# Optimization experiments

Measured on AMD Instinct MI355X. Metric: run time of the kernel, lower is better.

The kernel has to match this reference:

```python
import jax, jax.numpy as jnp
import numpy as np

B, N, C = 8, 16384, 80
MAX_OUT = 50
NEG = -1e30  # finite 'minus infinity' sentinel (safe under autodiff)


def setup_inputs() -> dict:
    key = jax.random.key(0)
    k1, k2 = jax.random.split(key)
    # two random corner points per box -> valid xyxy boxes in [0, 1000]
    pts = jax.random.uniform(k1, (B, N, 2, 2), dtype=jnp.float32) * 1000.0
    lo = jnp.min(pts, axis=2)
    hi = jnp.max(pts, axis=2)
    boxes = jnp.concatenate([lo, hi], axis=-1)  # [B, N, 4] (x1, y1, x2, y2)
    scores = jax.random.uniform(k2, (B, C, N), dtype=jnp.float32)
    return {
        "boxes": boxes,
        "scores": scores,
        "max_output_boxes_per_class": 50,
        "iou_threshold": jnp.array([0.5], dtype=jnp.float32),
        "score_threshold": jnp.array([0.5], dtype=jnp.float32),
    }


def _area(b):
    return (b[..., 2] - b[..., 0]) * (b[..., 3] - b[..., 1])


def _iou_one_vs_all(box, boxes):
    # box: [4], boxes: [N, 4] -> [N]
    x1 = jnp.maximum(box[0], boxes[:, 0])
    y1 = jnp.maximum(box[1], boxes[:, 1])
    x2 = jnp.minimum(box[2], boxes[:, 2])
    y2 = jnp.minimum(box[3], boxes[:, 3])
    inter = jnp.clip(x2 - x1, 0.0) * jnp.clip(y2 - y1, 0.0)
    union = _area(box) + _area(boxes) - inter
    return inter / jnp.maximum(union, 1e-9)


def _nms_single(boxes, scores, iou_thr, score_thr, max_out):
    # Greedy NMS for one (batch, class) lane. Returns [max_out] original box
    # indices in score-descending order, padded with -1.
    n = scores.shape[0]
    s0 = jnp.where(scores > score_thr, scores, NEG)  # score-threshold filter
    arange_n = jnp.arange(n)

    def step(s, _):
        idx = jnp.argmax(s)
        valid = s[idx] > (0.5 * NEG)  # any live candidate left?
        box = boxes[idx]
        iou = _iou_one_vs_all(box, boxes)
        sup = (iou > iou_thr) | (arange_n == idx)  # suppress overlaps + self
        s_new = jnp.where(valid & sup, NEG, s)
        return s_new, jnp.where(valid, idx, -1)

    _, idxs = jax.lax.scan(step, s0, None, length=max_out)
    return idxs  # [max_out] int32, -1 padded


def reference(boxes, scores, max_output_boxes_per_class, iou_threshold, score_threshold):
    b, c = scores.shape[0], scores.shape[1]
    iou_thr = iou_threshold[0]
    score_thr = score_threshold[0]
    max_out = int(max_output_boxes_per_class)

    per_class = lambda bx, sc: _nms_single(bx, sc, iou_thr, score_thr, max_out)
    nms_bc = jax.vmap(jax.vmap(per_class, in_axes=(None, 0)), in_axes=(0, 0))
    idxs = nms_bc(boxes, scores)  # [B, C, max_out]

    valid = idxs >= 0
    b_ids = jnp.broadcast_to(jnp.arange(b)[:, None, None], idxs.shape)
    c_ids = jnp.broadcast_to(jnp.arange(c)[None, :, None], idxs.shape)
    triples = jnp.stack(
        [jnp.where(valid, b_ids, -1), jnp.where(valid, c_ids, -1), idxs], axis=-1
    )
    # Padded equivalent of the dynamic [num_selected, 3] ONNX output:
    # rows with -1 are padding; valid rows are (batch, class, box) in the same
    # batch-major / class-major / score-descending order as the torch loop.
    return triples.reshape(-1, 3).astype(jnp.int64)
```

## Files before the change

### kernel.cpp

```cpp
#include <hip/hip_runtime.h>
#include <stdint.h>


#define NMS_B 8
#define NMS_N 16384
#define NMS_C 80
#define NMS_MAX_OUT 50
#define NTHREADS 256
#define NLANES (NMS_B * NMS_C)

#define OPT_THR 0.98828125f
#define FCAP 256
#define WMAX (FCAP / 64)
#define SPLIT 4
#define SEG 120
#define SCAN_N (NMS_N / SPLIT)

#define NBUCK 256
#define SCAP 1024
#define T_MIN 320

typedef unsigned long long u64;

#define WS_FLAGS  0
#define WS_CNTS   (NLANES * 4)
#define WS_TOTALS (WS_CNTS + NLANES * SPLIT * 4)
#define WS_KEYS   (WS_TOTALS + NLANES * SPLIT * 4)
#define WS_NEED   ((size_t)WS_KEYS + (size_t)NLANES * SPLIT * SEG * 8)

__device__ __forceinline__ float iou_exact(float4 A, float areaA, float4 Bx) {
    float x1 = fmaxf(A.x, Bx.x);
    float y1 = fmaxf(A.y, Bx.y);
    float x2 = fminf(A.z, Bx.z);
    float y2 = fminf(A.w, Bx.w);
    float dx = fmaxf(__fsub_rn(x2, x1), 0.0f);
    float dy = fmaxf(__fsub_rn(y2, y1), 0.0f);
    if (!(dx > 0.0f && dy > 0.0f)) return 0.0f;
    float inter = __fmul_rn(dx, dy);
    float areaB = __fmul_rn(__fsub_rn(Bx.z, Bx.x), __fsub_rn(Bx.w, Bx.y));
    float uni   = __fsub_rn(__fadd_rn(areaA, areaB), inter);
    return __fdiv_rn(inter, fmaxf(uni, 1e-9f));
}

__device__ __forceinline__ u64 umax64(u64 a, u64 b) { return a > b ? a : b; }
__device__ __forceinline__ u64 umin64(u64 a, u64 b) { return a < b ? a : b; }

__global__ __launch_bounds__(NTHREADS) void nms_scan(
    const float* __restrict__ scores,
    const float* __restrict__ p_sthr,
    int* __restrict__ cnts,
    int* __restrict__ totals,
    u64* __restrict__ keys)
{
    __shared__ u64 lkey[SEG];
    __shared__ int lcnt, ltot;

    const int bid  = blockIdx.x;
    const int bc   = bid / SPLIT;
    const int part = bid % SPLIT;
    const int tid  = threadIdx.x;

    const float4* sc4 = (const float4*)(scores + (size_t)bc * NMS_N + part * SCAN_N);
    float4 av[4];
    #pragma unroll
    for (int u = 0; u < 4; ++u) av[u] = sc4[u * NTHREADS + tid];
    __builtin_amdgcn_sched_barrier(0);

    if (tid == 0) { lcnt = 0; ltot = 0; }
    __syncthreads();

    const float sthr = p_sthr[0];
    int lt = 0;
    #pragma unroll
    for (int u = 0; u < 4; ++u) {
        const int i = u * NTHREADS + tid;
        float ss[4] = {av[u].x, av[u].y, av[u].z, av[u].w};
        #pragma unroll
        for (int j = 0; j < 4; ++j) {
            float s = ss[j];
            bool cand = (s > sthr);
            lt += cand ? 1 : 0;
            if (cand && s >= OPT_THR) {
                int n = part * SCAN_N + i * 4 + j;
                int p = atomicAdd(&lcnt, 1);
                if (p < SEG)
                    lkey[p] = ((u64)__float_as_uint(s) << 32)
                            | ((u64)(NMS_N - 1 - n) << 18);
            }
        }
    }
    #pragma unroll
    for (int off = 32; off > 0; off >>= 1) lt += __shfl_down(lt, off, 64);
    if ((tid & 63) == 0) atomicAdd(&ltot, lt);
    __syncthreads();

    const int cnt = lcnt;
    if (tid == 0) {
        cnts[bc * SPLIT + part]   = cnt;
        totals[bc * SPLIT + part] = ltot;
    }
    u64* kseg = keys + ((size_t)bc * SPLIT + part) * SEG;
    const int mm = (cnt < SEG) ? cnt : SEG;
    if (tid < mm) kseg[tid] = lkey[tid];
}

template <bool OUT64>
__global__ __launch_bounds__(64) void nms_sortwalk(
    const float* __restrict__ boxes,
    const int* __restrict__ p_maxout,
    const float* __restrict__ p_iou,
    void* __restrict__ out_raw,
    int* __restrict__ flags,
    const int* __restrict__ cnts,
    const int* __restrict__ totals,
    const u64* __restrict__ keys)
{
    __shared__ int    sn_[FCAP];
    __shared__ float4 sbox[FCAP];

    const int lane = threadIdx.x;
    const int bc   = blockIdx.x;
    const int b    = bc / NMS_C;
    const int c    = bc % NMS_C;

    const float iou_thr = p_iou[0];
    int maxo = p_maxout[0];
    if (maxo > NMS_MAX_OUT) maxo = NMS_MAX_OUT;
    if (maxo < 0) maxo = 0;

    int*       out32 = (int*)out_raw       + (size_t)bc * NMS_MAX_OUT * 3;
    long long* out64 = (long long*)out_raw + (size_t)bc * NMS_MAX_OUT * 3;
    #pragma unroll
    for (int i = lane; i < NMS_MAX_OUT * 3; i += 64) {
        if (OUT64) out64[i] = -1LL; else out32[i] = -1;
    }

    const int c0 = cnts[bc * SPLIT + 0], c1 = cnts[bc * SPLIT + 1];
    const int c2 = cnts[bc * SPLIT + 2], c3 = cnts[bc * SPLIT + 3];
    const int tt = totals[bc * SPLIT + 0] + totals[bc * SPLIT + 1]
                 + totals[bc * SPLIT + 2] + totals[bc * SPLIT + 3];
    const int o1 = c0, o2 = c0 + c1, o3 = c0 + c1 + c2;
    const int m  = o3 + c3;
    const bool bad = (c0 > SEG) | (c1 > SEG) | (c2 > SEG) | (c3 > SEG) | (m > FCAP);
    if (bad) {
        if (lane == 0) flags[bc] = 1;
        return;
    }
    const int rem = tt - m;

    const u64* kb = keys + (size_t)bc * SPLIT * SEG;
    u64 v[WMAX];
    #pragma unroll
    for (int q = 0; q < WMAX; ++q) {
        const int idx = q * 64 + lane;
        int p, base;
        if (idx < o1)      { p = 0; base = 0;  }
        else if (idx < o2) { p = 1; base = o1; }
        else if (idx < o3) { p = 2; base = o2; }
        else               { p = 3; base = o3; }
        v[q] = (idx < m) ? kb[(size_t)p * SEG + (idx - base)] : 0ull;
    }

    #define STAGE_SHFL(J, D0, D1, D2, D3) {                                       \
        const bool low_ = ((lane & (J)) == 0);                                    \
        { u64 o = __shfl_xor(v[0], (J), 64); bool d_ = (D0);                      \
          v[0] = (low_ == d_) ? umax64(v[0], o) : umin64(v[0], o); }              \
        { u64 o = __shfl_xor(v[1], (J), 64); bool d_ = (D1);                      \
          v[1] = (low_ == d_) ? umax64(v[1], o) : umin64(v[1], o); }              \
        { u64 o = __shfl_xor(v[2], (J), 64); bool d_ = (D2);                      \
          v[2] = (low_ == d_) ? umax64(v[2], o) : umin64(v[2], o); }              \
        { u64 o = __shfl_xor(v[3], (J), 64); bool d_ = (D3);                      \
          v[3] = (low_ == d_) ? umax64(v[3], o) : umin64(v[3], o); }              \
    }

    #pragma unroll
    for (int k = 2; k <= 32; k <<= 1) {
        #pragma unroll
        for (int j = k >> 1; j > 0; j >>= 1) {
            const bool dd = ((lane & k) == 0);
            STAGE_SHFL(j, dd, dd, dd, dd);
        }
    }
    #pragma unroll
    for (int j = 32; j > 0; j >>= 1) STAGE_SHFL(j, true, false, true, false);
    { u64 a = v[0], bb = v[1]; v[0] = umax64(a, bb); v[1] = umin64(a, bb); }
    { u64 a = v[2], bb = v[3]; v[2] = umin64(a, bb); v[3] = umax64(a, bb); }
    #pragma unroll
    for (int j = 32; j > 0; j >>= 1) STAGE_SHFL(j, true, true, false, false);
    { u64 a = v[0], bb = v[2]; v[0] = umax64(a, bb); v[2] = umin64(a, bb); }
    { u64 a = v[1], bb = v[3]; v[1] = umax64(a, bb); v[3] = umin64(a, bb); }
    { u64 a = v[0], bb = v[1]; v[0] = umax64(a, bb); v[1] = umin64(a, bb); }
    { u64 a = v[2], bb = v[3]; v[2] = umax64(a, bb); v[3] = umin64(a, bb); }
    #pragma unroll
    for (int j = 32; j > 0; j >>= 1) STAGE_SHFL(j, true, true, true, true);
    #undef STAGE_SHFL

    const float4* boxes_b = (const float4*)(boxes + (size_t)b * NMS_N * 4);
    #pragma unroll
    for (int q = 0; q < WMAX; ++q) {
        const int r = q * 64 + lane;
        const int n = NMS_N - 1 - (int)((v[q] >> 18) & 0x3FFFull);
        sn_[r] = n;
        sbox[r] = boxes_b[n];
    }

    float selx = 1e30f, sely = 1e30f, selz = -1e30f, selw = -1e30f, sela = 0.0f;
    int t = 0, r = 0, need_slow = 0;
    float4 cand = (m > 0) ? sbox[0] : make_float4(0.f, 0.f, 0.f, 0.f);

    while (t < maxo && r < m) {
        const int rn = (r + 1 < FCAP) ? (r + 1) : r;
        const float4 nxt = sbox[rn];

        const float areaC = __fmul_rn(__fsub_rn(cand.z, cand.x),
                                      __fsub_rn(cand.w, cand.y));
        float x1 = fmaxf(selx, cand.x);
        float y1 = fmaxf(sely, cand.y);
        float x2 = fminf(selz, cand.z);
        float y2 = fminf(selw, cand.w);
        float dx = fmaxf(__fsub_rn(x2, x1), 0.0f);
        float dy = fmaxf(__fsub_rn(y2, y1), 0.0f);
        bool sup = false;
        if (dx > 0.0f && dy > 0.0f) {
            float inter = __fmul_rn(dx, dy);
            float uni   = __fsub_rn(__fadd_rn(sela, areaC), inter);
            sup = __fdiv_rn(inter, fmaxf(uni, 1e-9f)) > iou_thr;
        }
        if (__ballot(sup) == 0ull) {
            if (lane == 0) {
                const int n = sn_[r];
                if (OUT64) {
                    out64[t * 3 + 0] = (long long)b;
                    out64[t * 3 + 1] = (long long)c;
                    out64[t * 3 + 2] = (long long)n;
                } else {
                    out32[t * 3 + 0] = b;
                    out32[t * 3 + 1] = c;
                    out32[t * 3 + 2] = n;
                }
            }
            if (lane == t) {
                selx = cand.x; sely = cand.y; selz = cand.z; selw = cand.w;
                sela = areaC;
            }
            ++t;
        }
        ++r;
        cand = nxt;
    }
    if (t < maxo && rem > 0) need_slow = 1;
    if (lane == 0) flags[bc] = need_slow;
}

template <bool OUT64>
__global__ __launch_bounds__(NTHREADS, 4) void nms_fast_mono(
    const float* __restrict__ boxes,
    const float* __restrict__ scores,
    const int* __restrict__ p_maxout,
    const float* __restrict__ p_iou,
    const float* __restrict__ p_sthr,
    void* __restrict__ out_raw,
    int* __restrict__ flags)
{
    __shared__ u64    skey[FCAP];
    __shared__ int    sn_[FCAP];
    __shared__ float4 sbox[FCAP];
    __shared__ int    s_cnt, s_total;

    const int tid = threadIdx.x;
    const int bc  = blockIdx.x;
    const int b   = bc / NMS_C;
    const int c   = bc % NMS_C;

    const float4* sc4     = (const float4*)(scores + ((size_t)b * NMS_C + c) * NMS_N);
    const float4* boxes_b = (const float4*)(boxes + (size_t)b * NMS_N * 4);

    float4 av[16];
    #pragma unroll
    for (int u = 0; u < 16; ++u) av[u] = sc4[u * NTHREADS + tid];
    __builtin_amdgcn_sched_barrier(0);

    const float score_thr = p_sthr[0];
    const float iou_thr   = p_iou[0];
    int maxo = p_maxout[0];
    if (maxo > NMS_MAX_OUT) maxo = NMS_MAX_OUT;
    if (maxo < 0) maxo = 0;

    int*       out32 = (int*)out_raw       + (size_t)bc * NMS_MAX_OUT * 3;
    long long* out64 = (long long*)out_raw + (size_t)bc * NMS_MAX_OUT * 3;
    for (int i = tid; i < NMS_MAX_OUT * 3; i += NTHREADS) {
        if (OUT64) out64[i] = -1LL; else out32[i] = -1;
    }

    if (tid == 0) { s_cnt = 0; s_total = 0; }
    __syncthreads();

    int local_total = 0;
    #pragma unroll
    for (int u = 0; u < 16; ++u) {
        const int i = u * NTHREADS + tid;
        float ss[4] = {av[u].x, av[u].y, av[u].z, av[u].w};
        #pragma unroll
        for (int j = 0; j < 4; ++j) {
            float s = ss[j];
            bool cand = (s > score_thr);
            local_total += cand ? 1 : 0;
            if (cand && s >= OPT_THR) {
                int n = i * 4 + j;
                int p = atomicAdd(&s_cnt, 1);
                if (p < FCAP) {
                    skey[p] = ((u64)__float_as_uint(s) << 32)
                            | ((u64)(NMS_N - 1 - n) << 18);
                }
            }
        }
    }
    atomicAdd(&s_total, local_total);
    __syncthreads();

    const int cn = s_cnt;
    const int m  = (cn < FCAP) ? cn : FCAP;
    if (cn > FCAP) {
        if (tid == 0) flags[bc] = 1;
        return;
    }
    if (tid >= 64) return;
    const int lane = tid;
    const int rem  = s_total - cn;

    u64 v[WMAX];
    #pragma unroll
    for (int q = 0; q < WMAX; ++q) {
        const int idx = q * 64 + lane;
        v[q] = (idx < m) ? skey[idx] : 0ull;
    }

    #define STAGE_SHFL(J, D0, D1, D2, D3) {                                       \
        const bool low_ = ((lane & (J)) == 0);                                    \
        { u64 o = __shfl_xor(v[0], (J), 64); bool d_ = (D0);                      \
          v[0] = (low_ == d_) ? umax64(v[0], o) : umin64(v[0], o); }              \
        { u64 o = __shfl_xor(v[1], (J), 64); bool d_ = (D1);                      \
          v[1] = (low_ == d_) ? umax64(v[1], o) : umin64(v[1], o); }              \
        { u64 o = __shfl_xor(v[2], (J), 64); bool d_ = (D2);                      \
          v[2] = (low_ == d_) ? umax64(v[2], o) : umin64(v[2], o); }              \
        { u64 o = __shfl_xor(v[3], (J), 64); bool d_ = (D3);                      \
          v[3] = (low_ == d_) ? umax64(v[3], o) : umin64(v[3], o); }              \
    }

    #pragma unroll
    for (int k = 2; k <= 32; k <<= 1) {
        #pragma unroll
        for (int j = k >> 1; j > 0; j >>= 1) {
            const bool dd = ((lane & k) == 0);
            STAGE_SHFL(j, dd, dd, dd, dd);
        }
    }
    #pragma unroll
    for (int j = 32; j > 0; j >>= 1) STAGE_SHFL(j, true, false, true, false);
    { u64 a = v[0], bb = v[1]; v[0] = umax64(a, bb); v[1] = umin64(a, bb); }
    { u64 a = v[2], bb = v[3]; v[2] = umin64(a, bb); v[3] = umax64(a, bb); }
    #pragma unroll
    for (int j = 32; j > 0; j >>= 1) STAGE_SHFL(j, true, true, false, false);
    { u64 a = v[0], bb = v[2]; v[0] = umax64(a, bb); v[2] = umin64(a, bb); }
    { u64 a = v[1], bb = v[3]; v[1] = umax64(a, bb); v[3] = umin64(a, bb); }
    { u64 a = v[0], bb = v[1]; v[0] = umax64(a, bb); v[1] = umin64(a, bb); }
    { u64 a = v[2], bb = v[3]; v[2] = umax64(a, bb); v[3] = umin64(a, bb); }
    #pragma unroll
    for (int j = 32; j > 0; j >>= 1) STAGE_SHFL(j, true, true, true, true);
    #undef STAGE_SHFL

    #pragma unroll
    for (int q = 0; q < WMAX; ++q) {
        const int r = q * 64 + lane;
        const int n = NMS_N - 1 - (int)((v[q] >> 18) & 0x3FFFull);
        sn_[r] = n;
        sbox[r] = boxes_b[n];
    }

    float selx = 1e30f, sely = 1e30f, selz = -1e30f, selw = -1e30f, sela = 0.0f;
    int t = 0, r = 0, need_slow = 0;
    float4 cand = (m > 0) ? sbox[0] : make_float4(0.f, 0.f, 0.f, 0.f);

    while (t < maxo && r < m) {
        const int rn = (r + 1 < FCAP) ? (r + 1) : r;
        const float4 nxt = sbox[rn];
        const float areaC = __fmul_rn(__fsub_rn(cand.z, cand.x),
                                      __fsub_rn(cand.w, cand.y));
        float x1 = fmaxf(selx, cand.x);
        float y1 = fmaxf(sely, cand.y);
        float x2 = fminf(selz, cand.z);
        float y2 = fminf(selw, cand.w);
        float dx = fmaxf(__fsub_rn(x2, x1), 0.0f);
        float dy = fmaxf(__fsub_rn(y2, y1), 0.0f);
        bool sup = false;
        if (dx > 0.0f && dy > 0.0f) {
            float inter = __fmul_rn(dx, dy);
            float uni   = __fsub_rn(__fadd_rn(sela, areaC), inter);
            sup = __fdiv_rn(inter, fmaxf(uni, 1e-9f)) > iou_thr;
        }
        if (__ballot(sup) == 0ull) {
            if (lane == 0) {
                const int n = sn_[r];
                if (OUT64) {
                    out64[t * 3 + 0] = (long long)b;
                    out64[t * 3 + 1] = (long long)c;
                    out64[t * 3 + 2] = (long long)n;
                } else {
                    out32[t * 3 + 0] = b;
                    out32[t * 3 + 1] = c;
                    out32[t * 3 + 2] = n;
                }
            }
            if (lane == t) {
                selx = cand.x; sely = cand.y; selz = cand.z; selw = cand.w;
                sela = areaC;
            }
            ++t;
        }
        ++r;
        cand = nxt;
    }
    if (t < maxo && rem > 0) need_slow = 1;
    if (lane == 0) flags[bc] = need_slow;
}

__device__ __forceinline__ int bucketf(float s) {
    int v = (int)__float_as_uint(s) - 0x3F000000;
    v >>= 15;
    return v < 0 ? 0 : (v > 255 ? 255 : v);
}

template <bool OUT64>
__global__ __launch_bounds__(NTHREADS) void nms_slow(
    const float* __restrict__ boxes,
    const float* __restrict__ scores,
    const int* __restrict__ p_maxout,
    const float* __restrict__ p_iou,
    const float* __restrict__ p_sthr,
    void* __restrict__ out_raw,
    const int* __restrict__ flags)
{
    __shared__ int    hist[NBUCK];
    __shared__ u64    key[SCAP];
    __shared__ float4 cbox[SCAP];
    __shared__ float4 selbox[NMS_MAX_OUT];
    __shared__ u64    s_wmax[NTHREADS / 64];
    __shared__ u64    s_best;
    __shared__ int    s_cnt, s_cutLo, s_cutHi, s_rem, s_state;

    const int tid = threadIdx.x;
    const int bc  = blockIdx.x;
    if (flags && flags[bc] == 0) return;
    const int b   = bc / NMS_C;
    const int c   = bc % NMS_C;

    const float score_thr = p_sthr[0];
    const float iou_thr   = p_iou[0];
    int maxo = p_maxout[0];
    if (maxo > NMS_MAX_OUT) maxo = NMS_MAX_OUT;
    if (maxo < 0) maxo = 0;

    int*       out32 = (int*)out_raw       + (size_t)bc * NMS_MAX_OUT * 3;
    long long* out64 = (long long*)out_raw + (size_t)bc * NMS_MAX_OUT * 3;
    for (int i = tid; i < NMS_MAX_OUT * 3; i += NTHREADS) {
        if (OUT64) out64[i] = -1LL; else out32[i] = -1;
    }

    const float*  sc      = scores + ((size_t)b * NMS_C + c) * NMS_N;
    const float4* sc4     = (const float4*)sc;
    const float4* boxes_b = (const float4*)(boxes + (size_t)b * NMS_N * 4);

    for (int i = tid; i < NBUCK; i += NTHREADS) hist[i] = 0;
    if (tid == 0) s_cnt = 0;
    __syncthreads();
    for (int i = tid; i < NMS_N / 4; i += NTHREADS) {
        float4 s4 = sc4[i];
        float ss[4] = {s4.x, s4.y, s4.z, s4.w};
        #pragma unroll
        for (int j = 0; j < 4; ++j)
            if (ss[j] > score_thr) atomicAdd(&hist[bucketf(ss[j])], 1);
    }
    __syncthreads();

    if (tid == 0) {
        int cum = 0, cut = NBUCK;
        for (int bk = NBUCK - 1; bk >= 0; --bk) {
            int h = hist[bk];
            if (cum > 0 && cum + h > SCAP) break;
            cum += h; cut = bk;
            if (cum >= T_MIN) break;
        }
        s_cutLo = cut; s_cutHi = NBUCK - 1;
        int rem = 0;
        for (int bk = 0; bk < cut; ++bk) rem += hist[bk];
        s_rem = rem;
    }
    __syncthreads();

    auto compact = [&](int lo, int hi) {
        for (int i = tid; i < NMS_N / 4; i += NTHREADS) {
            float4 s4 = sc4[i];
            float ss[4] = {s4.x, s4.y, s4.z, s4.w};
            #pragma unroll
            for (int j = 0; j < 4; ++j) {
                float s = ss[j];
                if (s > score_thr) {
                    int bk = bucketf(s);
                    if (bk >= lo && bk <= hi) {
                        int n = i * 4 + j;
                        int p = atomicAdd(&s_cnt, 1);
                        if (p < SCAP) {
                            key[p] = ((u64)__float_as_uint(s) << 24)
                                   | ((u64)(NMS_N - 1 - n) << 10)
                                   | (u64)p;
                            cbox[p] = boxes_b[n];
                        }
                    }
                }
            }
        }
    };
    compact(s_cutLo, s_cutHi);
    __syncthreads();

    int t = 0;
    while (t < maxo) {
        int m = s_cnt; if (m > SCAP) m = SCAP;
        u64 lmax = 0ull;
        for (int i = tid; i < m; i += NTHREADS) {
            u64 k = key[i];
            if (k > lmax) lmax = k;
        }
        #pragma unroll
        for (int off = 32; off > 0; off >>= 1) {
            u64 o = __shfl_down(lmax, off);
            if (o > lmax) lmax = o;
        }
        if ((tid & 63) == 0) s_wmax[tid >> 6] = lmax;
        __syncthreads();
        if (tid == 0) {
            u64 best = s_wmax[0];
            #pragma unroll
            for (int w = 1; w < NTHREADS / 64; ++w)
                if (s_wmax[w] > best) best = s_wmax[w];
            s_best = best;
            if (best) {
                int slot = (int)(best & 0x3FFull);
                int n    = NMS_N - 1 - (int)((best >> 10) & 0x3FFFull);
                key[slot] = 0ull;
                if (OUT64) {
                    out64[t * 3 + 0] = (long long)b;
                    out64[t * 3 + 1] = (long long)c;
                    out64[t * 3 + 2] = (long long)n;
                } else {
                    out32[t * 3 + 0] = b;
                    out32[t * 3 + 1] = c;
                    out32[t * 3 + 2] = n;
                }
                selbox[t] = cbox[slot];
                s_state = 0;
            } else if (s_rem == 0) {
                s_state = 2;
            } else {
                int hiB = s_cutLo - 1;
                int cum = 0, cut = hiB + 1;
                for (int bk = hiB; bk >= 0; --bk) {
                    int h = hist[bk];
                    if (cum > 0 && cum + h > SCAP) break;
                    cum += h; cut = bk;
                    if (cum >= T_MIN) break;
                }
                s_cutLo = cut; s_cutHi = hiB;
                int rem = 0;
                for (int bk = 0; bk < cut; ++bk) rem += hist[bk];
                s_rem = rem;
                s_cnt = 0;
                s_state = 1;
            }
        }
        __syncthreads();

        if (s_state == 2) break;

        if (s_state == 0) {
            const float4 A = selbox[t];
            const float areaA = __fmul_rn(__fsub_rn(A.z, A.x), __fsub_rn(A.w, A.y));
            int m0 = s_cnt; if (m0 > SCAP) m0 = SCAP;
            for (int i = tid; i < m0; i += NTHREADS) {
                u64 k = key[i];
                if (!k) continue;
                if (iou_exact(A, areaA, cbox[i]) > iou_thr) key[i] = 0ull;
            }
            __syncthreads();
            ++t;
        } else {
            compact(s_cutLo, s_cutHi);
            __syncthreads();
            int m2 = s_cnt; if (m2 > SCAP) m2 = SCAP;
            for (int i = tid; i < m2; i += NTHREADS) {
                u64 k = key[i];
                if (!k) continue;
                float4 Bx = cbox[i];
                for (int j = 0; j < t; ++j) {
                    float4 A = selbox[j];
                    float areaA = __fmul_rn(__fsub_rn(A.z, A.x), __fsub_rn(A.w, A.y));
                    if (iou_exact(A, areaA, Bx) > iou_thr) { key[i] = 0ull; break; }
                }
            }
            __syncthreads();
        }
    }
}

extern "C" void kernel_launch(void* const* d_in, const int* in_sizes, int n_in,
                              void* d_out, int out_size, void* d_ws, size_t ws_size,
                              hipStream_t stream) {
    const float* boxes  = (const float*)d_in[0];
    const float* scores = (const float*)d_in[1];
    const int*   p_maxo = (const int*)d_in[2];
    const float* p_iou  = (const float*)d_in[3];
    const float* p_sthr = (const float*)d_in[4];

    const dim3 block(NTHREADS);
    const bool out64 = (out_size == NLANES * NMS_MAX_OUT * 3 * 2);

    char* ws = (char*)d_ws;
    int*  flags  = (int*)(ws + WS_FLAGS);
    int*  cnts   = (int*)(ws + WS_CNTS);
    int*  totals = (int*)(ws + WS_TOTALS);
    u64*  keys   = (u64*)(ws + WS_KEYS);

    if (ws_size >= WS_NEED) {
        hipLaunchKernelGGL(nms_scan, dim3(NLANES * SPLIT), block, 0, stream,
                           scores, p_sthr, cnts, totals, keys);
        if (out64) {
            hipLaunchKernelGGL(nms_sortwalk<true>, dim3(NLANES), dim3(64), 0, stream,
                               boxes, p_maxo, p_iou, d_out, flags, cnts, totals, keys);
            hipLaunchKernelGGL(nms_slow<true>, dim3(NLANES), block, 0, stream,
                               boxes, scores, p_maxo, p_iou, p_sthr, d_out, flags);
        } else {
            hipLaunchKernelGGL(nms_sortwalk<false>, dim3(NLANES), dim3(64), 0, stream,
                               boxes, p_maxo, p_iou, d_out, flags, cnts, totals, keys);
            hipLaunchKernelGGL(nms_slow<false>, dim3(NLANES), block, 0, stream,
                               boxes, scores, p_maxo, p_iou, p_sthr, d_out, flags);
        }
    } else if (ws_size >= (size_t)NLANES * sizeof(int)) {
        if (out64) {
            hipLaunchKernelGGL(nms_fast_mono<true>, dim3(NLANES), block, 0, stream,
                               boxes, scores, p_maxo, p_iou, p_sthr, d_out, flags);
            hipLaunchKernelGGL(nms_slow<true>, dim3(NLANES), block, 0, stream,
                               boxes, scores, p_maxo, p_iou, p_sthr, d_out, flags);
        } else {
            hipLaunchKernelGGL(nms_fast_mono<false>, dim3(NLANES), block, 0, stream,
                               boxes, scores, p_maxo, p_iou, p_sthr, d_out, flags);
            hipLaunchKernelGGL(nms_slow<false>, dim3(NLANES), block, 0, stream,
                               boxes, scores, p_maxo, p_iou, p_sthr, d_out, flags);
        }
    } else {
        if (out64) {
            hipLaunchKernelGGL(nms_slow<true>, dim3(NLANES), block, 0, stream,
                               boxes, scores, p_maxo, p_iou, p_sthr, d_out, (const int*)nullptr);
        } else {
            hipLaunchKernelGGL(nms_slow<false>, dim3(NLANES), block, 0, stream,
                               boxes, scores, p_maxo, p_iou, p_sthr, d_out, (const int*)nullptr);
        }
    }
}
```

Baseline: 39.76 us.

## Fuse sort-walk and slow-path NMS kernels into one launch

Merges the per-lane sort/greedy-walk kernel and the fallback slow NMS kernel into a single fused kernel that calls a noinline slow_body device function when the fast path fails. This removes one kernel launch and the flag round trip through global memory. In exchange, the fused kernel runs with 256 threads per block, where the walk used 64, and it carries the slow path's larger shared-memory footprint, which may lower occupancy.

```diff
diff --git a/kernel.cpp b/kernel.cpp
--- a/kernel.cpp
+++ b/kernel.cpp
@@ -45,400 +45,21 @@
 __device__ __forceinline__ u64 umax64(u64 a, u64 b) { return a > b ? a : b; }
 __device__ __forceinline__ u64 umin64(u64 a, u64 b) { return a < b ? a : b; }
 
-__global__ __launch_bounds__(NTHREADS) void nms_scan(
-    const float* __restrict__ scores,
-    const float* __restrict__ p_sthr,
-    int* __restrict__ cnts,
-    int* __restrict__ totals,
-    u64* __restrict__ keys)
-{
-    __shared__ u64 lkey[SEG];
-    __shared__ int lcnt, ltot;
-
-    const int bid  = blockIdx.x;
-    const int bc   = bid / SPLIT;
-    const int part = bid % SPLIT;
-    const int tid  = threadIdx.x;
-
-    const float4* sc4 = (const float4*)(scores + (size_t)bc * NMS_N + part * SCAN_N);
-    float4 av[4];
-    #pragma unroll
-    for (int u = 0; u < 4; ++u) av[u] = sc4[u * NTHREADS + tid];
-    __builtin_amdgcn_sched_barrier(0);
-
-    if (tid == 0) { lcnt = 0; ltot = 0; }
-    __syncthreads();
-
-    const float sthr = p_sthr[0];
-    int lt = 0;
-    #pragma unroll
-    for (int u = 0; u < 4; ++u) {
-        const int i = u * NTHREADS + tid;
-        float ss[4] = {av[u].x, av[u].y, av[u].z, av[u].w};
-        #pragma unroll
-        for (int j = 0; j < 4; ++j) {
-            float s = ss[j];
-            bool cand = (s > sthr);
-            lt += cand ? 1 : 0;
-            if (cand && s >= OPT_THR) {
-                int n = part * SCAN_N + i * 4 + j;
-                int p = atomicAdd(&lcnt, 1);
-                if (p < SEG)
-                    lkey[p] = ((u64)__float_as_uint(s) << 32)
-                            | ((u64)(NMS_N - 1 - n) << 18);
-            }
-        }
-    }
-    #pragma unroll
-    for (int off = 32; off > 0; off >>= 1) lt += __shfl_down(lt, off, 64);
-    if ((tid & 63) == 0) atomicAdd(&ltot, lt);
-    __syncthreads();
-
-    const int cnt = lcnt;
-    if (tid == 0) {
-        cnts[bc * SPLIT + part]   = cnt;
-        totals[bc * SPLIT + part] = ltot;
-    }
-    u64* kseg = keys + ((size_t)bc * SPLIT + part) * SEG;
-    const int mm = (cnt < SEG) ? cnt : SEG;
-    if (tid < mm) kseg[tid] = lkey[tid];
+__device__ __forceinline__ int bucketf(float s) {
+    int v = (int)__float_as_uint(s) - 0x3F000000;
+    v >>= 15;
+    return v < 0 ? 0 : (v > 255 ? 255 : v);
 }
 
 template <bool OUT64>
-__global__ __launch_bounds__(64) void nms_sortwalk(
-    const float* __restrict__ boxes,
-    const int* __restrict__ p_maxout,
-    const float* __restrict__ p_iou,
-    void* __restrict__ out_raw,
-    int* __restrict__ flags,
-    const int* __restrict__ cnts,
-    const int* __restrict__ totals,
-    const u64* __restrict__ keys)
-{
-    __shared__ int    sn_[FCAP];
-    __shared__ float4 sbox[FCAP];
-
-    const int lane = threadIdx.x;
-    const int bc   = blockIdx.x;
-    const int b    = bc / NMS_C;
-    const int c    = bc % NMS_C;
-
-    const float iou_thr = p_iou[0];
-    int maxo = p_maxout[0];
-    if (maxo > NMS_MAX_OUT) maxo = NMS_MAX_OUT;
-    if (maxo < 0) maxo = 0;
-
-    int*       out32 = (int*)out_raw       + (size_t)bc * NMS_MAX_OUT * 3;
-    long long* out64 = (long long*)out_raw + (size_t)bc * NMS_MAX_OUT * 3;
-    #pragma unroll
-    for (int i = lane; i < NMS_MAX_OUT * 3; i += 64) {
-        if (OUT64) out64[i] = -1LL; else out32[i] = -1;
-    }
-
-    const int c0 = cnts[bc * SPLIT + 0], c1 = cnts[bc * SPLIT + 1];
-    const int c2 = cnts[bc * SPLIT + 2], c3 = cnts[bc * SPLIT + 3];
-    const int tt = totals[bc * SPLIT + 0] + totals[bc * SPLIT + 1]
-                 + totals[bc * SPLIT + 2] + totals[bc * SPLIT + 3];
-    const int o1 = c0, o2 = c0 + c1, o3 = c0 + c1 + c2;
-    const int m  = o3 + c3;
-    const bool bad = (c0 > SEG) | (c1 > SEG) | (c2 > SEG) | (c3 > SEG) | (m > FCAP);
-    if (bad) {
-        if (lane == 0) flags[bc] = 1;
-        return;
-    }
-    const int rem = tt - m;
-
-    const u64* kb = keys + (size_t)bc * SPLIT * SEG;
-    u64 v[WMAX];
-    #pragma unroll
-    for (int q = 0; q < WMAX; ++q) {
-        const int idx = q * 64 + lane;
-        int p, base;
-        if (idx < o1)      { p = 0; base = 0;  }
-        else if (idx < o2) { p = 1; base = o1; }
-        else if (idx < o3) { p = 2; base = o2; }
-        else               { p = 3; base = o3; }
-        v[q] = (idx < m) ? kb[(size_t)p * SEG + (idx - base)] : 0ull;
-    }
-
-    #define STAGE_SHFL(J, D0, D1, D2, D3) {                                       \
-        const bool low_ = ((lane & (J)) == 0);                                    \
-        { u64 o = __shfl_xor(v[0], (J), 64); bool d_ = (D0);                      \
-          v[0] = (low_ == d_) ? umax64(v[0], o) : umin64(v[0], o); }              \
-        { u64 o = __shfl_xor(v[1], (J), 64); bool d_ = (D1);                      \
-          v[1] = (low_ == d_) ? umax64(v[1], o) : umin64(v[1], o); }              \
-        { u64 o = __shfl_xor(v[2], (J), 64); bool d_ = (D2);                      \
-          v[2] = (low_ == d_) ? umax64(v[2], o) : umin64(v[2], o); }              \
-        { u64 o = __shfl_xor(v[3], (J), 64); bool d_ = (D3);                      \
-          v[3] = (low_ == d_) ? umax64(v[3], o) : umin64(v[3], o); }              \
-    }
-
-    #pragma unroll
-    for (int k = 2; k <= 32; k <<= 1) {
-        #pragma unroll
-        for (int j = k >> 1; j > 0; j >>= 1) {
-            const bool dd = ((lane & k) == 0);
-            STAGE_SHFL(j, dd, dd, dd, dd);
-        }
-    }
-    #pragma unroll
-    for (int j = 32; j > 0; j >>= 1) STAGE_SHFL(j, true, false, true, false);
-    { u64 a = v[0], bb = v[1]; v[0] = umax64(a, bb); v[1] = umin64(a, bb); }
-    { u64 a = v[2], bb = v[3]; v[2] = umin64(a, bb); v[3] = umax64(a, bb); }
-    #pragma unroll
-    for (int j = 32; j > 0; j >>= 1) STAGE_SHFL(j, true, true, false, false);
-    { u64 a = v[0], bb = v[2]; v[0] = umax64(a, bb); v[2] = umin64(a, bb); }
-    { u64 a = v[1], bb = v[3]; v[1] = umax64(a, bb); v[3] = umin64(a, bb); }
-    { u64 a = v[0], bb = v[1]; v[0] = umax64(a, bb); v[1] = umin64(a, bb); }
-    { u64 a = v[2], bb = v[3]; v[2] = umax64(a, bb); v[3] = umin64(a, bb); }
-    #pragma unroll
-    for (int j = 32; j > 0; j >>= 1) STAGE_SHFL(j, true, true, true, true);
-    #undef STAGE_SHFL
-
-    const float4* boxes_b = (const float4*)(boxes + (size_t)b * NMS_N * 4);
-    #pragma unroll
-    for (int q = 0; q < WMAX; ++q) {
-        const int r = q * 64 + lane;
-        const int n = NMS_N - 1 - (int)((v[q] >> 18) & 0x3FFFull);
-        sn_[r] = n;
-        sbox[r] = boxes_b[n];
-    }
-
-    float selx = 1e30f, sely = 1e30f, selz = -1e30f, selw = -1e30f, sela = 0.0f;
-    int t = 0, r = 0, need_slow = 0;
-    float4 cand = (m > 0) ? sbox[0] : make_float4(0.f, 0.f, 0.f, 0.f);
-
-    while (t < maxo && r < m) {
-        const int rn = (r + 1 < FCAP) ? (r + 1) : r;
-        const float4 nxt = sbox[rn];
-
-        const float areaC = __fmul_rn(__fsub_rn(cand.z, cand.x),
-                                      __fsub_rn(cand.w, cand.y));
-        float x1 = fmaxf(selx, cand.x);
-        float y1 = fmaxf(sely, cand.y);
-        float x2 = fminf(selz, cand.z);
-        float y2 = fminf(selw, cand.w);
-        float dx = fmaxf(__fsub_rn(x2, x1), 0.0f);
-        float dy = fmaxf(__fsub_rn(y2, y1), 0.0f);
-        bool sup = false;
-        if (dx > 0.0f && dy > 0.0f) {
-            float inter = __fmul_rn(dx, dy);
-            float uni   = __fsub_rn(__fadd_rn(sela, areaC), inter);
-            sup = __fdiv_rn(inter, fmaxf(uni, 1e-9f)) > iou_thr;
-        }
-        if (__ballot(sup) == 0ull) {
-            if (lane == 0) {
-                const int n = sn_[r];
-                if (OUT64) {
-                    out64[t * 3 + 0] = (long long)b;
-                    out64[t * 3 + 1] = (long long)c;
-                    out64[t * 3 + 2] = (long long)n;
-                } else {
-                    out32[t * 3 + 0] = b;
-                    out32[t * 3 + 1] = c;
-                    out32[t * 3 + 2] = n;
-                }
-            }
-            if (lane == t) {
-                selx = cand.x; sely = cand.y; selz = cand.z; selw = cand.w;
-                sela = areaC;
-            }
-            ++t;
-        }
-        ++r;
-        cand = nxt;
-    }
-    if (t < maxo && rem > 0) need_slow = 1;
-    if (lane == 0) flags[bc] = need_slow;
-}
-
-template <bool OUT64>
-__global__ __launch_bounds__(NTHREADS, 4) void nms_fast_mono(
+__device__ __noinline__ void slow_body(
     const float* __restrict__ boxes,
     const float* __restrict__ scores,
     const int* __restrict__ p_maxout,
     const float* __restrict__ p_iou,
     const float* __restrict__ p_sthr,
     void* __restrict__ out_raw,
-    int* __restrict__ flags)
-{
-    __shared__ u64    skey[FCAP];
-    __shared__ int    sn_[FCAP];
-    __shared__ float4 sbox[FCAP];
-    __shared__ int    s_cnt, s_total;
-
-    const int tid = threadIdx.x;
-    const int bc  = blockIdx.x;
-    const int b   = bc / NMS_C;
-    const int c   = bc % NMS_C;
-
-    const float4* sc4     = (const float4*)(scores + ((size_t)b * NMS_C + c) * NMS_N);
-    const float4* boxes_b = (const float4*)(boxes + (size_t)b * NMS_N * 4);
-
-    float4 av[16];
-    #pragma unroll
-    for (int u = 0; u < 16; ++u) av[u] = sc4[u * NTHREADS + tid];
-    __builtin_amdgcn_sched_barrier(0);
-
-    const float score_thr = p_sthr[0];
-    const float iou_thr   = p_iou[0];
-    int maxo = p_maxout[0];
-    if (maxo > NMS_MAX_OUT) maxo = NMS_MAX_OUT;
-    if (maxo < 0) maxo = 0;
-
-    int*       out32 = (int*)out_raw       + (size_t)bc * NMS_MAX_OUT * 3;
-    long long* out64 = (long long*)out_raw + (size_t)bc * NMS_MAX_OUT * 3;
-    for (int i = tid; i < NMS_MAX_OUT * 3; i += NTHREADS) {
-        if (OUT64) out64[i] = -1LL; else out32[i] = -1;
-    }
-
-    if (tid == 0) { s_cnt = 0; s_total = 0; }
-    __syncthreads();
-
-    int local_total = 0;
-    #pragma unroll
-    for (int u = 0; u < 16; ++u) {
-        const int i = u * NTHREADS + tid;
-        float ss[4] = {av[u].x, av[u].y, av[u].z, av[u].w};
-        #pragma unroll
-        for (int j = 0; j < 4; ++j) {
-            float s = ss[j];
-            bool cand = (s > score_thr);
-            local_total += cand ? 1 : 0;
-            if (cand && s >= OPT_THR) {
-                int n = i * 4 + j;
-                int p = atomicAdd(&s_cnt, 1);
-                if (p < FCAP) {
-                    skey[p] = ((u64)__float_as_uint(s) << 32)
-                            | ((u64)(NMS_N - 1 - n) << 18);
-                }
-            }
-        }
-    }
-    atomicAdd(&s_total, local_total);
-    __syncthreads();
-
-    const int cn = s_cnt;
-    const int m  = (cn < FCAP) ? cn : FCAP;
-    if (cn > FCAP) {
-        if (tid == 0) flags[bc] = 1;
-        return;
-    }
-    if (tid >= 64) return;
-    const int lane = tid;
-    const int rem  = s_total - cn;
-
-    u64 v[WMAX];
-    #pragma unroll
-    for (int q = 0; q < WMAX; ++q) {
-        const int idx = q * 64 + lane;
-        v[q] = (idx < m) ? skey[idx] : 0ull;
-    }
-
-    #define STAGE_SHFL(J, D0, D1, D2, D3) {                                       \
-        const bool low_ = ((lane & (J)) == 0);                                    \
-        { u64 o = __shfl_xor(v[0], (J), 64); bool d_ = (D0);                      \
-          v[0] = (low_ == d_) ? umax64(v[0], o) : umin64(v[0], o); }              \
-        { u64 o = __shfl_xor(v[1], (J), 64); bool d_ = (D1);                      \
-          v[1] = (low_ == d_) ? umax64(v[1], o) : umin64(v[1], o); }              \
-        { u64 o = __shfl_xor(v[2], (J), 64); bool d_ = (D2);                      \
-          v[2] = (low_ == d_) ? umax64(v[2], o) : umin64(v[2], o); }              \
-        { u64 o = __shfl_xor(v[3], (J), 64); bool d_ = (D3);                      \
-          v[3] = (low_ == d_) ? umax64(v[3], o) : umin64(v[3], o); }              \
-    }
-
-    #pragma unroll
-    for (int k = 2; k <= 32; k <<= 1) {
-        #pragma unroll
-        for (int j = k >> 1; j > 0; j >>= 1) {
-            const bool dd = ((lane & k) == 0);
-            STAGE_SHFL(j, dd, dd, dd, dd);
-        }
-    }
-    #pragma unroll
-    for (int j = 32; j > 0; j >>= 1) STAGE_SHFL(j, true, false, true, false);
-    { u64 a = v[0], bb = v[1]; v[0] = umax64(a, bb); v[1] = umin64(a, bb); }
-    { u64 a = v[2], bb = v[3]; v[2] = umin64(a, bb); v[3] = umax64(a, bb); }
-    #pragma unroll
-    for (int j = 32; j > 0; j >>= 1) STAGE_SHFL(j, true, true, false, false);
-    { u64 a = v[0], bb = v[2]; v[0] = umax64(a, bb); v[2] = umin64(a, bb); }
-    { u64 a = v[1], bb = v[3]; v[1] = umax64(a, bb); v[3] = umin64(a, bb); }
-    { u64 a = v[0], bb = v[1]; v[0] = umax64(a, bb); v[1] = umin64(a, bb); }
-    { u64 a = v[2], bb = v[3]; v[2] = umax64(a, bb); v[3] = umin64(a, bb); }
-    #pragma unroll
-    for (int j = 32; j > 0; j >>= 1) STAGE_SHFL(j, true, true, true, true);
-    #undef STAGE_SHFL
-
-    #pragma unroll
-    for (int q = 0; q < WMAX; ++q) {
-        const int r = q * 64 + lane;
-        const int n = NMS_N - 1 - (int)((v[q] >> 18) & 0x3FFFull);
-        sn_[r] = n;
-        sbox[r] = boxes_b[n];
-    }
-
-    float selx = 1e30f, sely = 1e30f, selz = -1e30f, selw = -1e30f, sela = 0.0f;
-    int t = 0, r = 0, need_slow = 0;
-    float4 cand = (m > 0) ? sbox[0] : make_float4(0.f, 0.f, 0.f, 0.f);
-
-    while (t < maxo && r < m) {
-        const int rn = (r + 1 < FCAP) ? (r + 1) : r;
-        const float4 nxt = sbox[rn];
-        const float areaC = __fmul_rn(__fsub_rn(cand.z, cand.x),
-                                      __fsub_rn(cand.w, cand.y));
-        float x1 = fmaxf(selx, cand.x);
-        float y1 = fmaxf(sely, cand.y);
-        float x2 = fminf(selz, cand.z);
-        float y2 = fminf(selw, cand.w);
-        float dx = fmaxf(__fsub_rn(x2, x1), 0.0f);
-        float dy = fmaxf(__fsub_rn(y2, y1), 0.0f);
-        bool sup = false;
-        if (dx > 0.0f && dy > 0.0f) {
-            float inter = __fmul_rn(dx, dy);
-            float uni   = __fsub_rn(__fadd_rn(sela, areaC), inter);
-            sup = __fdiv_rn(inter, fmaxf(uni, 1e-9f)) > iou_thr;
-        }
-        if (__ballot(sup) == 0ull) {
-            if (lane == 0) {
-                const int n = sn_[r];
-                if (OUT64) {
-                    out64[t * 3 + 0] = (long long)b;
-                    out64[t * 3 + 1] = (long long)c;
-                    out64[t * 3 + 2] = (long long)n;
-                } else {
-                    out32[t * 3 + 0] = b;
-                    out32[t * 3 + 1] = c;
-                    out32[t * 3 + 2] = n;
-                }
-            }
-            if (lane == t) {
-                selx = cand.x; sely = cand.y; selz = cand.z; selw = cand.w;
-                sela = areaC;
-            }
-            ++t;
-        }
-        ++r;
-        cand = nxt;
-    }
-    if (t < maxo && rem > 0) need_slow = 1;
-    if (lane == 0) flags[bc] = need_slow;
-}
-
-__device__ __forceinline__ int bucketf(float s) {
-    int v = (int)__float_as_uint(s) - 0x3F000000;
-    v >>= 15;
-    return v < 0 ? 0 : (v > 255 ? 255 : v);
-}
-
-template <bool OUT64>
-__global__ __launch_bounds__(NTHREADS) void nms_slow(
-    const float* __restrict__ boxes,
-    const float* __restrict__ scores,
-    const int* __restrict__ p_maxout,
-    const float* __restrict__ p_iou,
-    const float* __restrict__ p_sthr,
-    void* __restrict__ out_raw,
-    const int* __restrict__ flags)
+    int bc)
 {
     __shared__ int    hist[NBUCK];
     __shared__ u64    key[SCAP];
@@ -449,8 +70,6 @@
     __shared__ int    s_cnt, s_cutLo, s_cutHi, s_rem, s_state;
 
     const int tid = threadIdx.x;
-    const int bc  = blockIdx.x;
-    if (flags && flags[bc] == 0) return;
     const int b   = bc / NMS_C;
     const int c   = bc % NMS_C;
 
@@ -612,6 +231,407 @@
     }
 }
 
+__global__ __launch_bounds__(NTHREADS) void nms_scan(
+    const float* __restrict__ scores,
+    const float* __restrict__ p_sthr,
+    int* __restrict__ cnts,
+    int* __restrict__ totals,
+    u64* __restrict__ keys)
+{
+    __shared__ u64 lkey[SEG];
+    __shared__ int lcnt, ltot;
+
+    const int bid  = blockIdx.x;
+    const int bc   = bid / SPLIT;
+    const int part = bid % SPLIT;
+    const int tid  = threadIdx.x;
+
+    const float4* sc4 = (const float4*)(scores + (size_t)bc * NMS_N + part * SCAN_N);
+    float4 av[4];
+    #pragma unroll
+    for (int u = 0; u < 4; ++u) av[u] = sc4[u * NTHREADS + tid];
+    __builtin_amdgcn_sched_barrier(0);
+
+    if (tid == 0) { lcnt = 0; ltot = 0; }
+    __syncthreads();
+
+    const float sthr = p_sthr[0];
+    int lt = 0;
+    #pragma unroll
+    for (int u = 0; u < 4; ++u) {
+        const int i = u * NTHREADS + tid;
+        float ss[4] = {av[u].x, av[u].y, av[u].z, av[u].w};
+        #pragma unroll
+        for (int j = 0; j < 4; ++j) {
+            float s = ss[j];
+            bool cand = (s > sthr);
+            lt += cand ? 1 : 0;
+            if (cand && s >= OPT_THR) {
+                int n = part * SCAN_N + i * 4 + j;
+                int p = atomicAdd(&lcnt, 1);
+                if (p < SEG)
+                    lkey[p] = ((u64)__float_as_uint(s) << 32)
+                            | ((u64)(NMS_N - 1 - n) << 18);
+            }
+        }
+    }
+    #pragma unroll
+    for (int off = 32; off > 0; off >>= 1) lt += __shfl_down(lt, off, 64);
+    if ((tid & 63) == 0) atomicAdd(&ltot, lt);
+    __syncthreads();
+
+    const int cnt = lcnt;
+    if (tid == 0) {
+        cnts[bc * SPLIT + part]   = cnt;
+        totals[bc * SPLIT + part] = ltot;
+    }
+    u64* kseg = keys + ((size_t)bc * SPLIT + part) * SEG;
+    const int mm = (cnt < SEG) ? cnt : SEG;
+    if (tid < mm) kseg[tid] = lkey[tid];
+}
+
+template <bool OUT64>
+__global__ __launch_bounds__(NTHREADS) void nms_fused(
+    const float* __restrict__ boxes,
+    const float* __restrict__ scores,
+    const int* __restrict__ p_maxout,
+    const float* __restrict__ p_iou,
+    const float* __restrict__ p_sthr,
+    void* __restrict__ out_raw,
+    const int* __restrict__ cnts,
+    const int* __restrict__ totals,
+    const u64* __restrict__ keys)
+{
+    __shared__ int    sn_[FCAP];
+    __shared__ float4 sbox[FCAP];
+    __shared__ int    s_need_slow;
+
+    const int tid  = threadIdx.x;
+    const int bc   = blockIdx.x;
+    const int b    = bc / NMS_C;
+    const int c    = bc % NMS_C;
+
+    const float iou_thr = p_iou[0];
+    int maxo = p_maxout[0];
+    if (maxo > NMS_MAX_OUT) maxo = NMS_MAX_OUT;
+    if (maxo < 0) maxo = 0;
+
+    int*       out32 = (int*)out_raw       + (size_t)bc * NMS_MAX_OUT * 3;
+    long long* out64 = (long long*)out_raw + (size_t)bc * NMS_MAX_OUT * 3;
+    for (int i = tid; i < NMS_MAX_OUT * 3; i += NTHREADS) {
+        if (OUT64) out64[i] = -1LL; else out32[i] = -1;
+    }
+
+    const int c0 = cnts[bc * SPLIT + 0], c1 = cnts[bc * SPLIT + 1];
+    const int c2 = cnts[bc * SPLIT + 2], c3 = cnts[bc * SPLIT + 3];
+    const int tt = totals[bc * SPLIT + 0] + totals[bc * SPLIT + 1]
+                 + totals[bc * SPLIT + 2] + totals[bc * SPLIT + 3];
+    const int o1 = c0, o2 = c0 + c1, o3 = c0 + c1 + c2;
+    const int m  = o3 + c3;
+    const bool bad = (c0 > SEG) | (c1 > SEG) | (c2 > SEG) | (c3 > SEG) | (m > FCAP);
+    if (bad) {
+        slow_body<OUT64>(boxes, scores, p_maxout, p_iou, p_sthr, out_raw, bc);
+        return;
+    }
+    const int rem = tt - m;
+
+    if (tid < 64) {
+        const int lane = tid;
+
+        const u64* kb = keys + (size_t)bc * SPLIT * SEG;
+        u64 v[WMAX];
+        #pragma unroll
+        for (int q = 0; q < WMAX; ++q) {
+            const int idx = q * 64 + lane;
+            int p, base;
+            if (idx < o1)      { p = 0; base = 0;  }
+            else if (idx < o2) { p = 1; base = o1; }
+            else if (idx < o3) { p = 2; base = o2; }
+            else               { p = 3; base = o3; }
+            v[q] = (idx < m) ? kb[(size_t)p * SEG + (idx - base)] : 0ull;
+        }
+
+        #define STAGE_SHFL(J, D0, D1, D2, D3) {                                   \
+            const bool low_ = ((lane & (J)) == 0);                                \
+            { u64 o = __shfl_xor(v[0], (J), 64); bool d_ = (D0);                  \
+              v[0] = (low_ == d_) ? umax64(v[0], o) : umin64(v[0], o); }          \
+            { u64 o = __shfl_xor(v[1], (J), 64); bool d_ = (D1);                  \
+              v[1] = (low_ == d_) ? umax64(v[1], o) : umin64(v[1], o); }          \
+            { u64 o = __shfl_xor(v[2], (J), 64); bool d_ = (D2);                  \
+              v[2] = (low_ == d_) ? umax64(v[2], o) : umin64(v[2], o); }          \
+            { u64 o = __shfl_xor(v[3], (J), 64); bool d_ = (D3);                  \
+              v[3] = (low_ == d_) ? umax64(v[3], o) : umin64(v[3], o); }          \
+        }
+
+        #pragma unroll
+        for (int k = 2; k <= 32; k <<= 1) {
+            #pragma unroll
+            for (int j = k >> 1; j > 0; j >>= 1) {
+                const bool dd = ((lane & k) == 0);
+                STAGE_SHFL(j, dd, dd, dd, dd);
+            }
+        }
+        #pragma unroll
+        for (int j = 32; j > 0; j >>= 1) STAGE_SHFL(j, true, false, true, false);
+        { u64 a = v[0], bb = v[1]; v[0] = umax64(a, bb); v[1] = umin64(a, bb); }
+        { u64 a = v[2], bb = v[3]; v[2] = umin64(a, bb); v[3] = umax64(a, bb); }
+        #pragma unroll
+        for (int j = 32; j > 0; j >>= 1) STAGE_SHFL(j, true, true, false, false);
+        { u64 a = v[0], bb = v[2]; v[0] = umax64(a, bb); v[2] = umin64(a, bb); }
+        { u64 a = v[1], bb = v[3]; v[1] = umax64(a, bb); v[3] = umin64(a, bb); }
+        { u64 a = v[0], bb = v[1]; v[0] = umax64(a, bb); v[1] = umin64(a, bb); }
+        { u64 a = v[2], bb = v[3]; v[2] = umax64(a, bb); v[3] = umin64(a, bb); }
+        #pragma unroll
+        for (int j = 32; j > 0; j >>= 1) STAGE_SHFL(j, true, true, true, true);
+        #undef STAGE_SHFL
+
+        const float4* boxes_b = (const float4*)(boxes + (size_t)b * NMS_N * 4);
+        #pragma unroll
+        for (int q = 0; q < WMAX; ++q) {
+            const int r = q * 64 + lane;
+            const int n = NMS_N - 1 - (int)((v[q] >> 18) & 0x3FFFull);
+            sn_[r] = n;
+            sbox[r] = boxes_b[n];
+        }
+
+        float selx = 1e30f, sely = 1e30f, selz = -1e30f, selw = -1e30f, sela = 0.0f;
+        int t = 0, r = 0;
+        float4 cand = (m > 0) ? sbox[0] : make_float4(0.f, 0.f, 0.f, 0.f);
+
+        while (t < maxo && r < m) {
+            const int rn = (r + 1 < FCAP) ? (r + 1) : r;
+            const float4 nxt = sbox[rn];
+
+            const float areaC = __fmul_rn(__fsub_rn(cand.z, cand.x),
+                                          __fsub_rn(cand.w, cand.y));
+            float x1 = fmaxf(selx, cand.x);
+            float y1 = fmaxf(sely, cand.y);
+            float x2 = fminf(selz, cand.z);
+            float y2 = fminf(selw, cand.w);
+            float dx = fmaxf(__fsub_rn(x2, x1), 0.0f);
+            float dy = fmaxf(__fsub_rn(y2, y1), 0.0f);
+            bool sup = false;
+            if (dx > 0.0f && dy > 0.0f) {
+                float inter = __fmul_rn(dx, dy);
+                float uni   = __fsub_rn(__fadd_rn(sela, areaC), inter);
+                sup = __fdiv_rn(inter, fmaxf(uni, 1e-9f)) > iou_thr;
+            }
+            if (__ballot(sup) == 0ull) {
+                if (lane == 0) {
+                    const int n = sn_[r];
+                    if (OUT64) {
+                        out64[t * 3 + 0] = (long long)b;
+                        out64[t * 3 + 1] = (long long)c;
+                        out64[t * 3 + 2] = (long long)n;
+                    } else {
+                        out32[t * 3 + 0] = b;
+                        out32[t * 3 + 1] = c;
+                        out32[t * 3 + 2] = n;
+                    }
+                }
+                if (lane == t) {
+                    selx = cand.x; sely = cand.y; selz = cand.z; selw = cand.w;
+                    sela = areaC;
+                }
+                ++t;
+            }
+            ++r;
+            cand = nxt;
+        }
+        if (lane == 0) s_need_slow = (t < maxo && rem > 0) ? 1 : 0;
+    }
+    __syncthreads();
+    if (s_need_slow)
+        slow_body<OUT64>(boxes, scores, p_maxout, p_iou, p_sthr, out_raw, bc);
+}
+
+template <bool OUT64>
+__global__ __launch_bounds__(NTHREADS, 4) void nms_fast_mono(
+    const float* __restrict__ boxes,
+    const float* __restrict__ scores,
+    const int* __restrict__ p_maxout,
+    const float* __restrict__ p_iou,
+    const float* __restrict__ p_sthr,
+    void* __restrict__ out_raw,
+    int* __restrict__ flags)
+{
+    __shared__ u64    skey[FCAP];
+    __shared__ int    sn_[FCAP];
+    __shared__ float4 sbox[FCAP];
+    __shared__ int    s_cnt, s_total;
+
+    const int tid = threadIdx.x;
+    const int bc  = blockIdx.x;
+    const int b   = bc / NMS_C;
+    const int c   = bc % NMS_C;
+
+    const float4* sc4     = (const float4*)(scores + ((size_t)b * NMS_C + c) * NMS_N);
+    const float4* boxes_b = (const float4*)(boxes + (size_t)b * NMS_N * 4);
+
+    float4 av[16];
+    #pragma unroll
+    for (int u = 0; u < 16; ++u) av[u] = sc4[u * NTHREADS + tid];
+    __builtin_amdgcn_sched_barrier(0);
+
+    const float score_thr = p_sthr[0];
+    const float iou_thr   = p_iou[0];
+    int maxo = p_maxout[0];
+    if (maxo > NMS_MAX_OUT) maxo = NMS_MAX_OUT;
+    if (maxo < 0) maxo = 0;
+
+    int*       out32 = (int*)out_raw       + (size_t)bc * NMS_MAX_OUT * 3;
+    long long* out64 = (long long*)out_raw + (size_t)bc * NMS_MAX_OUT * 3;
+    for (int i = tid; i < NMS_MAX_OUT * 3; i += NTHREADS) {
+        if (OUT64) out64[i] = -1LL; else out32[i] = -1;
+    }
+
+    if (tid == 0) { s_cnt = 0; s_total = 0; }
+    __syncthreads();
+
+    int local_total = 0;
+    #pragma unroll
+    for (int u = 0; u < 16; ++u) {
+        const int i = u * NTHREADS + tid;
+        float ss[4] = {av[u].x, av[u].y, av[u].z, av[u].w};
+        #pragma unroll
+        for (int j = 0; j < 4; ++j) {
+            float s = ss[j];
+            bool cand = (s > score_thr);
+            local_total += cand ? 1 : 0;
+            if (cand && s >= OPT_THR) {
+                int n = i * 4 + j;
+                int p = atomicAdd(&s_cnt, 1);
+                if (p < FCAP) {
+                    skey[p] = ((u64)__float_as_uint(s) << 32)
+                            | ((u64)(NMS_N - 1 - n) << 18);
+                }
+            }
+        }
+    }
+    atomicAdd(&s_total, local_total);
+    __syncthreads();
+
+    const int cn = s_cnt;
+    const int m  = (cn < FCAP) ? cn : FCAP;
+    if (cn > FCAP) {
+        if (tid == 0) flags[bc] = 1;
+        return;
+    }
+    if (tid >= 64) return;
+    const int lane = tid;
+    const int rem  = s_total - cn;
+
+    u64 v[WMAX];
+    #pragma unroll
+    for (int q = 0; q < WMAX; ++q) {
+        const int idx = q * 64 + lane;
+        v[q] = (idx < m) ? skey[idx] : 0ull;
+    }
+
+    #define STAGE_SHFL(J, D0, D1, D2, D3) {                                       \
+        const bool low_ = ((lane & (J)) == 0);                                    \
+        { u64 o = __shfl_xor(v[0], (J), 64); bool d_ = (D0);                      \
+          v[0] = (low_ == d_) ? umax64(v[0], o) : umin64(v[0], o); }              \
+        { u64 o = __shfl_xor(v[1], (J), 64); bool d_ = (D1);                      \
+          v[1] = (low_ == d_) ? umax64(v[1], o) : umin64(v[1], o); }              \
+        { u64 o = __shfl_xor(v[2], (J), 64); bool d_ = (D2);                      \
+          v[2] = (low_ == d_) ? umax64(v[2], o) : umin64(v[2], o); }              \
+        { u64 o = __shfl_xor(v[3], (J), 64); bool d_ = (D3);                      \
+          v[3] = (low_ == d_) ? umax64(v[3], o) : umin64(v[3], o); }              \
+    }
+
+    #pragma unroll
+    for (int k = 2; k <= 32; k <<= 1) {
+        #pragma unroll
+        for (int j = k >> 1; j > 0; j >>= 1) {
+            const bool dd = ((lane & k) == 0);
+            STAGE_SHFL(j, dd, dd, dd, dd);
+        }
+    }
+    #pragma unroll
+    for (int j = 32; j > 0; j >>= 1) STAGE_SHFL(j, true, false, true, false);
+    { u64 a = v[0], bb = v[1]; v[0] = umax64(a, bb); v[1] = umin64(a, bb); }
+    { u64 a = v[2], bb = v[3]; v[2] = umin64(a, bb); v[3] = umax64(a, bb); }
+    #pragma unroll
+    for (int j = 32; j > 0; j >>= 1) STAGE_SHFL(j, true, true, false, false);
+    { u64 a = v[0], bb = v[2]; v[0] = umax64(a, bb); v[2] = umin64(a, bb); }
+    { u64 a = v[1], bb = v[3]; v[1] = umax64(a, bb); v[3] = umin64(a, bb); }
+    { u64 a = v[0], bb = v[1]; v[0] = umax64(a, bb); v[1] = umin64(a, bb); }
+    { u64 a = v[2], bb = v[3]; v[2] = umax64(a, bb); v[3] = umin64(a, bb); }
+    #pragma unroll
+    for (int j = 32; j > 0; j >>= 1) STAGE_SHFL(j, true, true, true, true);
+    #undef STAGE_SHFL
+
+    #pragma unroll
+    for (int q = 0; q < WMAX; ++q) {
+        const int r = q * 64 + lane;
+        const int n = NMS_N - 1 - (int)((v[q] >> 18) & 0x3FFFull);
+        sn_[r] = n;
+        sbox[r] = boxes_b[n];
+    }
+
+    float selx = 1e30f, sely = 1e30f, selz = -1e30f, selw = -1e30f, sela = 0.0f;
+    int t = 0, r = 0, need_slow = 0;
+    float4 cand = (m > 0) ? sbox[0] : make_float4(0.f, 0.f, 0.f, 0.f);
+
+    while (t < maxo && r < m) {
+        const int rn = (r + 1 < FCAP) ? (r + 1) : r;
+        const float4 nxt = sbox[rn];
+        const float areaC = __fmul_rn(__fsub_rn(cand.z, cand.x),
+                                      __fsub_rn(cand.w, cand.y));
+        float x1 = fmaxf(selx, cand.x);
+        float y1 = fmaxf(sely, cand.y);
+        float x2 = fminf(selz, cand.z);
+        float y2 = fminf(selw, cand.w);
+        float dx = fmaxf(__fsub_rn(x2, x1), 0.0f);
+        float dy = fmaxf(__fsub_rn(y2, y1), 0.0f);
+        bool sup = false;
+        if (dx > 0.0f && dy > 0.0f) {
+            float inter = __fmul_rn(dx, dy);
+            float uni   = __fsub_rn(__fadd_rn(sela, areaC), inter);
+            sup = __fdiv_rn(inter, fmaxf(uni, 1e-9f)) > iou_thr;
+        }
+        if (__ballot(sup) == 0ull) {
+            if (lane == 0) {
+                const int n = sn_[r];
+                if (OUT64) {
+                    out64[t * 3 + 0] = (long long)b;
+                    out64[t * 3 + 1] = (long long)c;
+                    out64[t * 3 + 2] = (long long)n;
+                } else {
+                    out32[t * 3 + 0] = b;
+                    out32[t * 3 + 1] = c;
+                    out32[t * 3 + 2] = n;
+                }
+            }
+            if (lane == t) {
+                selx = cand.x; sely = cand.y; selz = cand.z; selw = cand.w;
+                sela = areaC;
+            }
+            ++t;
+        }
+        ++r;
+        cand = nxt;
+    }
+    if (t < maxo && rem > 0) need_slow = 1;
+    if (lane == 0) flags[bc] = need_slow;
+}
+
+template <bool OUT64>
+__global__ __launch_bounds__(NTHREADS) void nms_slow(
+    const float* __restrict__ boxes,
+    const float* __restrict__ scores,
+    const int* __restrict__ p_maxout,
+    const float* __restrict__ p_iou,
+    const float* __restrict__ p_sthr,
+    void* __restrict__ out_raw,
+    const int* __restrict__ flags)
+{
+    const int bc = blockIdx.x;
+    if (flags && flags[bc] == 0) return;
+    slow_body<OUT64>(boxes, scores, p_maxout, p_iou, p_sthr, out_raw, bc);
+}
+
 extern "C" void kernel_launch(void* const* d_in, const int* in_sizes, int n_in,
                               void* d_out, int out_size, void* d_ws, size_t ws_size,
                               hipStream_t stream) {
@@ -634,15 +654,13 @@
         hipLaunchKernelGGL(nms_scan, dim3(NLANES * SPLIT), block, 0, stream,
                            scores, p_sthr, cnts, totals, keys);
         if (out64) {
-            hipLaunchKernelGGL(nms_sortwalk<true>, dim3(NLANES), dim3(64), 0, stream,
-                               boxes, p_maxo, p_iou, d_out, flags, cnts, totals, keys);
-            hipLaunchKernelGGL(nms_slow<true>, dim3(NLANES), block, 0, stream,
-                               boxes, scores, p_maxo, p_iou, p_sthr, d_out, flags);
+            hipLaunchKernelGGL(nms_fused<true>, dim3(NLANES), block, 0, stream,
+                               boxes, scores, p_maxo, p_iou, p_sthr, d_out,
+                               cnts, totals, keys);
         } else {
-            hipLaunchKernelGGL(nms_sortwalk<false>, dim3(NLANES), dim3(64), 0, stream,
-                               boxes, p_maxo, p_iou, d_out, flags, cnts, totals, keys);
-            hipLaunchKernelGGL(nms_slow<false>, dim3(NLANES), block, 0, stream,
-                               boxes, scores, p_maxo, p_iou, p_sthr, d_out, flags);
+            hipLaunchKernelGGL(nms_fused<false>, dim3(NLANES), block, 0, stream,
+                               boxes, scores, p_maxo, p_iou, p_sthr, d_out,
+                               cnts, totals, keys);
         }
     } else if (ws_size >= (size_t)NLANES * sizeof(int)) {
         if (out64) {
```

Measured after the change: 38.30 us, median of 2. 3.7% less time.
